# Kernel tuning notes

Measured on AMD Instinct MI355X. Metric: run time of the kernel, lower is better.

Reference implementation:

```python
import jax, jax.numpy as jnp
import numpy as np

NUM_EMBEDDINGS = 2048
EMBEDDING_DIM = 512
INPUT_DIM = 256  # input_chan**2 = 16**2
COMMITMENT_COST = 0.25
BN_EPS = 1e-5


def setup_inputs() -> dict:
    key = jax.random.key(0)
    ks = jax.random.split(key, 8)
    B, N = 64, 1024
    inputs = jax.random.normal(ks[0], (B, N, INPUT_DIM), dtype=jnp.float32)
    # embedding init: uniform(-1/K, 1/K) as in the torch module
    emb_scale = 1.0 / NUM_EMBEDDINGS
    embedding = jax.random.uniform(ks[1], (NUM_EMBEDDINGS, EMBEDDING_DIM), dtype=jnp.float32,
                                   minval=-emb_scale, maxval=emb_scale)
    # Linear layers use torch convention W[out, in]
    W1 = jax.random.normal(ks[2], (EMBEDDING_DIM, INPUT_DIM), dtype=jnp.float32) / np.sqrt(INPUT_DIM)
    b1 = jnp.zeros((EMBEDDING_DIM,), dtype=jnp.float32)
    W2 = jax.random.normal(ks[3], (INPUT_DIM, EMBEDDING_DIM), dtype=jnp.float32) / np.sqrt(EMBEDDING_DIM)
    b2 = jnp.zeros((INPUT_DIM,), dtype=jnp.float32)
    # BatchNorm affine params initialized to 1/0 as in the module
    bn1_gamma = jnp.ones((INPUT_DIM,), dtype=jnp.float32)
    bn1_beta = jnp.zeros((INPUT_DIM,), dtype=jnp.float32)
    bn2_gamma = jnp.ones((EMBEDDING_DIM,), dtype=jnp.float32)
    bn2_beta = jnp.zeros((EMBEDDING_DIM,), dtype=jnp.float32)
    return {"inputs": inputs, "bn1_gamma": bn1_gamma, "bn1_beta": bn1_beta,
            "W1": W1, "b1": b1, "embedding": embedding,
            "bn2_gamma": bn2_gamma, "bn2_beta": bn2_beta, "W2": W2, "b2": b2}


def reference(inputs, bn1_gamma, bn1_beta, W1, b1, embedding, bn2_gamma, bn2_beta, W2, b2):
    sg = jax.lax.stop_gradient
    input_shape = inputs.shape
    flat = inputs.reshape(-1, INPUT_DIM)  # [T, D_in]
    # BatchNorm1d in eval mode (running_mean=0, running_var=1); Dropout is identity in eval.
    bn1_scale = 1.0 / jnp.sqrt(1.0 + BN_EPS)
    x = flat * (bn1_gamma * bn1_scale) + bn1_beta
    x = x @ W1.T + b1  # [T, E]
    # pairwise squared distances to codebook, argmin
    distances = (jnp.sum(x * x, axis=1, keepdims=True)
                 + jnp.sum(embedding * embedding, axis=1)
                 - 2.0 * x @ embedding.T)  # [T, K]
    encoding_indices = jnp.argmin(distances, axis=1)  # [T]
    # gather == one-hot @ embedding (same math, same gradient scatter-add)
    quantized = jnp.take(embedding, encoding_indices, axis=0)  # [T, E]
    bn2_scale = 1.0 / jnp.sqrt(1.0 + BN_EPS)
    quantized = quantized * (bn2_gamma * bn2_scale) + bn2_beta
    quantized = (quantized @ W2.T + b2).reshape(input_shape)
    e_latent_loss = jnp.mean((sg(quantized) - inputs) ** 2)
    q_latent_loss = jnp.mean((quantized - sg(inputs)) ** 2)
    loss = q_latent_loss + COMMITMENT_COST * e_latent_loss
    quantized_st = inputs + sg(quantized - inputs)  # straight-through
    T = flat.shape[0]
    usage = jnp.zeros((NUM_EMBEDDINGS,), dtype=jnp.float32).at[encoding_indices].add(1.0) / T
    return (loss, quantized_st, usage)
```

## Files before the change

### kernel.cpp

```cpp
#include <hip/hip_runtime.h>
#include <math.h>
#include <stdint.h>

#define TOK 65536
#define DIN 256
#define EDIM 512
#define KCB 2048
#define NTA 4096
#define NTB 128

#define OFF_MP   0u
#define OFF_CP   524288u
#define OFF_Q    526336u
#define OFF_W2T  1050624u
#define OFF_U    1181696u
#define OFF_CQ   1182208u
#define OFF_IDX  1182464u
#define OFF_AH   1248000u
#define OFF_BH   5442304u
#define TOT_F    5704448u

typedef short short8 __attribute__((ext_vector_type(8)));
typedef float f32x4 __attribute__((ext_vector_type(4)));

__device__ __forceinline__ unsigned short bf16rne(float x) {
    uint32_t u = __float_as_uint(x);
    u += 0x7fffu + ((u >> 16) & 1u);
    return (unsigned short)(u >> 16);
}
__device__ __forceinline__ void async_load16(const void* g, void* l) {
    __builtin_amdgcn_global_load_lds((const __attribute__((address_space(1))) void*)g,
                                     (__attribute__((address_space(3))) void*)l, 16, 0, 0);
}

__global__ void prep1_kernel(const float* __restrict__ W1, const float* __restrict__ W2,
                             const float* __restrict__ bn1_beta, const float* __restrict__ bn2_gamma,
                             const float* __restrict__ bn2_beta, const float* __restrict__ b2,
                             float* __restrict__ W2T, float* __restrict__ u, float* __restrict__ cQ,
                             float* __restrict__ out) {
    __shared__ float red[256];
    const int b = blockIdx.x, t = threadIdx.x;
    const int gid = b * 256 + t;
    if (gid == 0) out[0] = 0.0f;
    if (gid < KCB) out[1 + TOK * DIN + gid] = 0.0f;
    const float s = 1.0f / sqrtf(1.0f + 1e-5f);
    if (b < EDIM) {
        int e = b;
        W2T[e * DIN + t] = bn2_gamma[e] * s * W2[t * EDIM + e];
        float v = bn1_beta[t] * W1[e * DIN + t];
        red[t] = v; __syncthreads();
        for (int off = 128; off; off >>= 1) { if (t < off) red[t] += red[t + off]; __syncthreads(); }
        if (t == 0) u[e] = red[0];
    } else {
        int o = b - EDIM;
        float v = bn2_beta[t] * W2[o * EDIM + t] + bn2_beta[t + 256] * W2[o * EDIM + t + 256];
        red[t] = v; __syncthreads();
        for (int off = 128; off; off >>= 1) { if (t < off) red[t] += red[t + off]; __syncthreads(); }
        if (t == 0) cQ[o] = b2[o] + red[0];
    }
}

__global__ __launch_bounds__(256) void prep2_kernel(const float* __restrict__ E, const float* __restrict__ W1,
                                                    const float* __restrict__ W2T, const float* __restrict__ bn1_gamma,
                                                    const float* __restrict__ cQ,
                                                    float* __restrict__ Mp, float* __restrict__ Q) {
    __shared__ float Elds[4 * EDIM];
    const int k0 = blockIdx.x * 4, t = threadIdx.x;
    const float4* src = (const float4*)(E + (size_t)k0 * EDIM);
    float4* dst = (float4*)Elds;
    dst[t] = src[t];
    dst[256 + t] = src[256 + t];
    __syncthreads();
    float m[4] = {0, 0, 0, 0};
    float q[4] = {0, 0, 0, 0};
    for (int e0 = 0; e0 < EDIM; e0 += 8) {
        float w1v[8], w2v[8];
#pragma unroll
        for (int j = 0; j < 8; j++) {
            w1v[j] = W1[(e0 + j) * DIN + t];
            w2v[j] = W2T[(e0 + j) * DIN + t];
        }
#pragma unroll
        for (int j = 0; j < 8; j++) {
#pragma unroll
            for (int r = 0; r < 4; r++) {
                float ev = Elds[r * EDIM + e0 + j];
                m[r] += ev * w1v[j]; q[r] += ev * w2v[j];
            }
        }
    }
    const float s = 1.0f / sqrtf(1.0f + 1e-5f);
    const float gs = bn1_gamma[t] * s;
    const float cq = cQ[t];
#pragma unroll
    for (int r = 0; r < 4; r++) {
        Mp[(size_t)(k0 + r) * DIN + t] = gs * m[r];
        Q[(size_t)(k0 + r) * DIN + t] = q[r] + cq;
    }
}

__global__ __launch_bounds__(256) void prep3_packB_kernel(const float* __restrict__ E, const float* __restrict__ b1,
                                                          const float* __restrict__ u, float* __restrict__ cp,
                                                          const float* __restrict__ Mp,
                                                          unsigned short* __restrict__ Bh) {
    __shared__ __align__(16) unsigned short Hs[32 * 264];
    const int t = threadIdx.x, lane = t & 63;
    {
        const int k = blockIdx.x * 4 + (t >> 6);
        const float4* er = (const float4*)(E + (size_t)k * EDIM);
        float sa = 0.0f, sb = 0.0f;
#pragma unroll
        for (int i = 0; i < 2; i++) {
            int j4 = lane * 2 + i;
            float4 ev = er[j4];
            int e = j4 * 4;
            sa += ev.x * (b1[e] + u[e]) + ev.y * (b1[e + 1] + u[e + 1])
                + ev.z * (b1[e + 2] + u[e + 2]) + ev.w * (b1[e + 3] + u[e + 3]);
            sb += ev.x * ev.x + ev.y * ev.y + ev.z * ev.z + ev.w * ev.w;
        }
        float v = sa - 0.5f * sb;
#pragma unroll
        for (int off = 32; off; off >>= 1) v += __shfl_down(v, off, 64);
        if (lane == 0) cp[k] = v;
    }
    if (blockIdx.x >= 64) return;
    const int r0 = blockIdx.x * 32;
    const float4* src = (const float4*)(Mp + (size_t)r0 * DIN);
#pragma unroll
    for (int i = 0; i < 8; i++) {
        int id = i * 256 + t;
        int row = id >> 6, c4 = id & 63;
        float4 v = src[id];
        float f[4] = {v.x, v.y, v.z, v.w};
        ushort4 H;
        unsigned short* hp = (unsigned short*)&H;
#pragma unroll
        for (int j = 0; j < 4; j++) hp[j] = bf16rne(f[j]);
        *(ushort4*)&Hs[row * 264 + c4 * 4] = H;
    }
    __syncthreads();
    const int w = t >> 6;
#pragma unroll
    for (int q = 0; q < 4; q++) {
        int fb = q * 4 + w;
        int tl = fb >> 3, kc = fb & 7;
        int srow = tl * 16 + (lane & 15);
        int scol = kc * 32 + (lane >> 4) * 8;
        short8 vh = *(const short8*)&Hs[srow * 264 + scol];
        size_t off = ((size_t)kc * NTB + (r0 >> 4) + tl) * 512 + lane * 8;
        *(short8*)&Bh[off] = vh;
    }
}

__global__ __launch_bounds__(256) void packA_kernel(const float* __restrict__ X,
                                                    unsigned short* __restrict__ Hp) {
    __shared__ __align__(16) unsigned short Hs[32 * 264];
    const int t = threadIdx.x;
    const int r0 = blockIdx.x * 32;
    const float4* src = (const float4*)(X + (size_t)r0 * DIN);
#pragma unroll
    for (int i = 0; i < 8; i++) {
        int id = i * 256 + t;
        int row = id >> 6, c4 = id & 63;
        float4 v = src[id];
        float f[4] = {v.x, v.y, v.z, v.w};
        ushort4 H;
        unsigned short* hp = (unsigned short*)&H;
#pragma unroll
        for (int j = 0; j < 4; j++) hp[j] = bf16rne(f[j]);
        *(ushort4*)&Hs[row * 264 + c4 * 4] = H;
    }
    __syncthreads();
    const int lane = t & 63, w = t >> 6;
#pragma unroll
    for (int q = 0; q < 4; q++) {
        int fb = q * 4 + w;
        int tl = fb >> 3, kc = fb & 7;
        int srow = tl * 16 + (lane & 15);
        int scol = kc * 32 + (lane >> 4) * 8;
        short8 vh = *(const short8*)&Hs[srow * 264 + scol];
        size_t off = ((size_t)kc * NTA + (r0 >> 4) + tl) * 512 + lane * 8;
        *(short8*)&Hp[off] = vh;
    }
}

__global__ __launch_bounds__(256) void score_mfma_kernel(const unsigned short* __restrict__ Ah,
                                                         const unsigned short* __restrict__ Bh,
                                                         const float* __restrict__ cp,
                                                         int* __restrict__ idxOut) {
    __shared__ __align__(16) unsigned short Blds[2][16 * 512];
    const int t = threadIdx.x, lane = t & 63, w = t >> 6;
    const int m0 = blockIdx.x * 128;
    const int mt0 = (m0 >> 4) + w * 2;
    const int fr = lane & 15;
    const short8* A8 = (const short8*)Ah;

    short8 af[8][2];
#pragma unroll
    for (int kc = 0; kc < 8; kc++)
#pragma unroll
        for (int mt = 0; mt < 2; mt++)
            af[kc][mt] = A8[((size_t)kc * NTA + mt0 + mt) * 64 + lane];

#pragma unroll
    for (int i = 0; i < 4; i++) {
        int tl = i * 4 + w;
        int kc = tl >> 1, nt = tl & 1;
        async_load16(Bh + ((size_t)kc * NTB + nt) * 512 + lane * 8,
                     &Blds[0][tl * 512 + lane * 8]);
    }
    __syncthreads();

    float bestv[2][4];
    int besti[2][4];
#pragma unroll
    for (int mt = 0; mt < 2; mt++)
#pragma unroll
        for (int r = 0; r < 4; r++) { bestv[mt][r] = -3.4e38f; besti[mt][r] = 0; }

#pragma unroll 1
    for (int s = 0; s < 64; s++) {
        const int cur = s & 1;
        if (s < 63) {
            const int nxt = cur ^ 1;
#pragma unroll
            for (int i = 0; i < 4; i++) {
                int tl = i * 4 + w;
                int kc = tl >> 1, nt = tl & 1;
                async_load16(Bh + ((size_t)kc * NTB + (s + 1) * 2 + nt) * 512 + lane * 8,
                             &Blds[nxt][tl * 512 + lane * 8]);
            }
        }
        f32x4 acc[2][2];
#pragma unroll
        for (int mt = 0; mt < 2; mt++)
#pragma unroll
            for (int nt = 0; nt < 2; nt++) acc[mt][nt] = (f32x4){0.f, 0.f, 0.f, 0.f};
#pragma unroll
        for (int kc = 0; kc < 8; kc++) {
            short8 bf0 = *(const short8*)&Blds[cur][(kc * 2 + 0) * 512 + lane * 8];
            short8 bf1 = *(const short8*)&Blds[cur][(kc * 2 + 1) * 512 + lane * 8];
            acc[0][0] = __builtin_amdgcn_mfma_f32_16x16x32_bf16(af[kc][0], bf0, acc[0][0], 0, 0, 0);
            acc[0][1] = __builtin_amdgcn_mfma_f32_16x16x32_bf16(af[kc][0], bf1, acc[0][1], 0, 0, 0);
            acc[1][0] = __builtin_amdgcn_mfma_f32_16x16x32_bf16(af[kc][1], bf0, acc[1][0], 0, 0, 0);
            acc[1][1] = __builtin_amdgcn_mfma_f32_16x16x32_bf16(af[kc][1], bf1, acc[1][1], 0, 0, 0);
        }
        float cpv0 = cp[s * 32 + fr];
        float cpv1 = cp[s * 32 + 16 + fr];
#pragma unroll
        for (int mt = 0; mt < 2; mt++)
#pragma unroll
            for (int r = 0; r < 4; r++) {
                float bv = acc[mt][0][r] + cpv0;
                int bc = s * 32 + fr;
                float v1 = acc[mt][1][r] + cpv1;
                if (v1 > bv) { bv = v1; bc = s * 32 + 16 + fr; }
                if (bv > bestv[mt][r]) { bestv[mt][r] = bv; besti[mt][r] = bc; }
            }
        __syncthreads();
    }
#pragma unroll
    for (int mt = 0; mt < 2; mt++)
#pragma unroll
        for (int r = 0; r < 4; r++) {
            float bv = bestv[mt][r];
            int bc = besti[mt][r];
#pragma unroll
            for (int xm = 1; xm < 16; xm <<= 1) {
                float ov = __shfl_xor(bv, xm, 64);
                int oc = __shfl_xor(bc, xm, 64);
                if (ov > bv || (ov == bv && oc < bc)) { bv = ov; bc = oc; }
            }
            if (fr == 0) {
                int row = m0 + (w * 2 + mt) * 16 + (lane >> 4) * 4 + r;
                idxOut[row] = bc;
            }
        }
}

__global__ __launch_bounds__(256) void gather_out_kernel(const float* __restrict__ flat,
                                                         const float* __restrict__ Q,
                                                         const int* __restrict__ idx,
                                                         float* __restrict__ out) {
    const int t = threadIdx.x;
    const int lane = t & 63;
    const int gw = blockIdx.x * 4 + (t >> 6);
    float lsum = 0.0f;
    for (int r = 0; r < 16; r++) {
        int row = gw * 16 + r;
        int k = idx[row];
        const float* qr = Q + (size_t)k * DIN;
        const float* xr = flat + (size_t)row * DIN;
        float* ob = out + 1 + (size_t)row * DIN;
#pragma unroll
        for (int cc = 0; cc < 4; cc++) {
            int j = lane + 64 * cc;
            float q = qr[j];
            float d = q - xr[j];
            lsum += d * d;
            ob[j] = q;
        }
        if (lane == 0) atomicAdd(out + 1 + TOK * DIN + k, 1.0f / (float)TOK);
    }
#pragma unroll
    for (int off = 32; off; off >>= 1) lsum += __shfl_down(lsum, off, 64);
    if (lane == 0) atomicAdd(out, lsum * (1.25f / (float)((size_t)TOK * DIN)));
}

extern "C" void kernel_launch(void* const* d_in, const int* in_sizes, int n_in,
                              void* d_out, int out_size, void* d_ws, size_t ws_size,
                              hipStream_t stream) {
    const float* inputs = (const float*)d_in[0];
    const float* bn1_gamma = (const float*)d_in[1];
    const float* bn1_beta  = (const float*)d_in[2];
    const float* W1 = (const float*)d_in[3];
    const float* b1 = (const float*)d_in[4];
    const float* E  = (const float*)d_in[5];
    const float* bn2_gamma = (const float*)d_in[6];
    const float* bn2_beta  = (const float*)d_in[7];
    const float* W2 = (const float*)d_in[8];
    const float* b2 = (const float*)d_in[9];

    float* ws = (float*)d_ws;
    float* Mp  = ws + OFF_MP;
    float* cp  = ws + OFF_CP;
    float* Q   = ws + OFF_Q;
    float* W2T = ws + OFF_W2T;
    float* u   = ws + OFF_U;
    float* cQ  = ws + OFF_CQ;
    int* idx   = (int*)(ws + OFF_IDX);
    unsigned short* Ah = (unsigned short*)(ws + OFF_AH);
    unsigned short* Bh = (unsigned short*)(ws + OFF_BH);
    float* out = (float*)d_out;

    hipLaunchKernelGGL(packA_kernel, dim3(TOK / 32), dim3(256), 0, stream, inputs, Ah);
    hipLaunchKernelGGL(prep1_kernel, dim3(768), dim3(256), 0, stream,
                       W1, W2, bn1_beta, bn2_gamma, bn2_beta, b2, W2T, u, cQ, out);
    hipLaunchKernelGGL(prep2_kernel, dim3(512), dim3(256), 0, stream,
                       E, W1, W2T, bn1_gamma, cQ, Mp, Q);
    hipLaunchKernelGGL(prep3_packB_kernel, dim3(512), dim3(256), 0, stream,
                       E, b1, u, cp, Mp, Bh);
    hipLaunchKernelGGL(score_mfma_kernel, dim3(512), dim3(256), 0, stream,
                       Ah, Bh, cp, idx);
    hipLaunchKernelGGL(gather_out_kernel, dim3(1024), dim3(256), 0, stream,
                       inputs, Q, idx, out);
}
```

Baseline: 320.1 us.

## Fuse A packing and gather/loss into the score kernel, widen codebook tile

Removes the separate packA pass by converting each block's input rows to bf16 fragments directly in registers inside the score kernel. The gather/loss/usage step now runs inside the same kernel, with selected indices kept in shared memory. This avoids writing and re-reading the packed A buffer and the index buffer, and drops two launches. The score loop now handles 64 codebook entries per stage instead of 32, which doubles the shared-memory B buffer. Computing cp is merged into prep2 and packB runs as its own small kernel. The trade-off is more registers and LDS per block, which can lower occupancy, and the tail gather loop runs serially after the GEMM.

```diff
diff --git a/kernel.cpp b/kernel.cpp
--- a/kernel.cpp
+++ b/kernel.cpp
@@ -6,7 +6,6 @@
 #define DIN 256
 #define EDIM 512
 #define KCB 2048
-#define NTA 4096
 #define NTB 128
 
 #define OFF_MP   0u
@@ -15,10 +14,8 @@
 #define OFF_W2T  1050624u
 #define OFF_U    1181696u
 #define OFF_CQ   1182208u
-#define OFF_IDX  1182464u
-#define OFF_AH   1248000u
-#define OFF_BH   5442304u
-#define TOT_F    5704448u
+#define OFF_BH   1182464u
+#define TOT_F    1444608u
 
 typedef short short8 __attribute__((ext_vector_type(8)));
 typedef float f32x4 __attribute__((ext_vector_type(4)));
@@ -62,8 +59,10 @@
 
 __global__ __launch_bounds__(256) void prep2_kernel(const float* __restrict__ E, const float* __restrict__ W1,
                                                     const float* __restrict__ W2T, const float* __restrict__ bn1_gamma,
-                                                    const float* __restrict__ cQ,
-                                                    float* __restrict__ Mp, float* __restrict__ Q) {
+                                                    const float* __restrict__ cQ, const float* __restrict__ b1,
+                                                    const float* __restrict__ u,
+                                                    float* __restrict__ Mp, float* __restrict__ Q,
+                                                    float* __restrict__ cp) {
     __shared__ float Elds[4 * EDIM];
     const int k0 = blockIdx.x * 4, t = threadIdx.x;
     const float4* src = (const float4*)(E + (size_t)k0 * EDIM);
@@ -97,33 +96,25 @@
         Mp[(size_t)(k0 + r) * DIN + t] = gs * m[r];
         Q[(size_t)(k0 + r) * DIN + t] = q[r] + cq;
     }
-}
-
-__global__ __launch_bounds__(256) void prep3_packB_kernel(const float* __restrict__ E, const float* __restrict__ b1,
-                                                          const float* __restrict__ u, float* __restrict__ cp,
-                                                          const float* __restrict__ Mp,
-                                                          unsigned short* __restrict__ Bh) {
+    const int r = t >> 6, l = t & 63;
+    float sa = 0.0f, sb = 0.0f;
+#pragma unroll
+    for (int i = 0; i < 8; i++) {
+        int e = l + i * 64;
+        float ev = Elds[r * EDIM + e];
+        float be = b1[e] + u[e];
+        sa += ev * be; sb += ev * ev;
+    }
+    float v = sa - 0.5f * sb;
+#pragma unroll
+    for (int off = 32; off; off >>= 1) v += __shfl_down(v, off, 64);
+    if (l == 0) cp[k0 + r] = v;
+}
+
+__global__ __launch_bounds__(256) void packB_kernel(const float* __restrict__ Mp,
+                                                    unsigned short* __restrict__ Bh) {
     __shared__ __align__(16) unsigned short Hs[32 * 264];
-    const int t = threadIdx.x, lane = t & 63;
-    {
-        const int k = blockIdx.x * 4 + (t >> 6);
-        const float4* er = (const float4*)(E + (size_t)k * EDIM);
-        float sa = 0.0f, sb = 0.0f;
-#pragma unroll
-        for (int i = 0; i < 2; i++) {
-            int j4 = lane * 2 + i;
-            float4 ev = er[j4];
-            int e = j4 * 4;
-            sa += ev.x * (b1[e] + u[e]) + ev.y * (b1[e + 1] + u[e + 1])
-                + ev.z * (b1[e + 2] + u[e + 2]) + ev.w * (b1[e + 3] + u[e + 3]);
-            sb += ev.x * ev.x + ev.y * ev.y + ev.z * ev.z + ev.w * ev.w;
-        }
-        float v = sa - 0.5f * sb;
-#pragma unroll
-        for (int off = 32; off; off >>= 1) v += __shfl_down(v, off, 64);
-        if (lane == 0) cp[k] = v;
-    }
-    if (blockIdx.x >= 64) return;
+    const int t = threadIdx.x, lane = t & 63, w = t >> 6;
     const int r0 = blockIdx.x * 32;
     const float4* src = (const float4*)(Mp + (size_t)r0 * DIN);
 #pragma unroll
@@ -139,7 +130,6 @@
         *(ushort4*)&Hs[row * 264 + c4 * 4] = H;
     }
     __syncthreads();
-    const int w = t >> 6;
 #pragma unroll
     for (int q = 0; q < 4; q++) {
         int fb = q * 4 + w;
@@ -152,60 +142,36 @@
     }
 }
 
-__global__ __launch_bounds__(256) void packA_kernel(const float* __restrict__ X,
-                                                    unsigned short* __restrict__ Hp) {
-    __shared__ __align__(16) unsigned short Hs[32 * 264];
-    const int t = threadIdx.x;
-    const int r0 = blockIdx.x * 32;
-    const float4* src = (const float4*)(X + (size_t)r0 * DIN);
-#pragma unroll
-    for (int i = 0; i < 8; i++) {
-        int id = i * 256 + t;
-        int row = id >> 6, c4 = id & 63;
-        float4 v = src[id];
-        float f[4] = {v.x, v.y, v.z, v.w};
-        ushort4 H;
-        unsigned short* hp = (unsigned short*)&H;
-#pragma unroll
-        for (int j = 0; j < 4; j++) hp[j] = bf16rne(f[j]);
-        *(ushort4*)&Hs[row * 264 + c4 * 4] = H;
-    }
-    __syncthreads();
-    const int lane = t & 63, w = t >> 6;
-#pragma unroll
-    for (int q = 0; q < 4; q++) {
-        int fb = q * 4 + w;
-        int tl = fb >> 3, kc = fb & 7;
-        int srow = tl * 16 + (lane & 15);
-        int scol = kc * 32 + (lane >> 4) * 8;
-        short8 vh = *(const short8*)&Hs[srow * 264 + scol];
-        size_t off = ((size_t)kc * NTA + (r0 >> 4) + tl) * 512 + lane * 8;
-        *(short8*)&Hp[off] = vh;
-    }
-}
-
-__global__ __launch_bounds__(256) void score_mfma_kernel(const unsigned short* __restrict__ Ah,
-                                                         const unsigned short* __restrict__ Bh,
-                                                         const float* __restrict__ cp,
-                                                         int* __restrict__ idxOut) {
-    __shared__ __align__(16) unsigned short Blds[2][16 * 512];
+__global__ __launch_bounds__(256) void score_fused_kernel(const float* __restrict__ flat,
+                                                          const unsigned short* __restrict__ Bh,
+                                                          const float* __restrict__ cp,
+                                                          const float* __restrict__ Q,
+                                                          float* __restrict__ out) {
+    __shared__ __align__(16) unsigned short Blds[2][32 * 512];
+    __shared__ int ksel[128];
     const int t = threadIdx.x, lane = t & 63, w = t >> 6;
     const int m0 = blockIdx.x * 128;
-    const int mt0 = (m0 >> 4) + w * 2;
-    const int fr = lane & 15;
-    const short8* A8 = (const short8*)Ah;
+    const int fr = lane & 15, qr = lane >> 4;
 
     short8 af[8][2];
 #pragma unroll
     for (int kc = 0; kc < 8; kc++)
 #pragma unroll
-        for (int mt = 0; mt < 2; mt++)
-            af[kc][mt] = A8[((size_t)kc * NTA + mt0 + mt) * 64 + lane];
-
-#pragma unroll
-    for (int i = 0; i < 4; i++) {
+        for (int mt = 0; mt < 2; mt++) {
+            int row = m0 + w * 32 + mt * 16 + fr;
+            const float* p = flat + (size_t)row * DIN + kc * 32 + qr * 8;
+            float4 a = *(const float4*)p;
+            float4 b = *(const float4*)(p + 4);
+            float f[8] = {a.x, a.y, a.z, a.w, b.x, b.y, b.z, b.w};
+            unsigned short* hp = (unsigned short*)&af[kc][mt];
+#pragma unroll
+            for (int j = 0; j < 8; j++) hp[j] = bf16rne(f[j]);
+        }
+
+#pragma unroll
+    for (int i = 0; i < 8; i++) {
         int tl = i * 4 + w;
-        int kc = tl >> 1, nt = tl & 1;
+        int kc = tl >> 2, nt = tl & 3;
         async_load16(Bh + ((size_t)kc * NTB + nt) * 512 + lane * 8,
                      &Blds[0][tl * 512 + lane * 8]);
     }
@@ -218,47 +184,66 @@
 #pragma unroll
         for (int r = 0; r < 4; r++) { bestv[mt][r] = -3.4e38f; besti[mt][r] = 0; }
 
+    const f32x4 ZERO4 = {0.f, 0.f, 0.f, 0.f};
+
 #pragma unroll 1
-    for (int s = 0; s < 64; s++) {
+    for (int s = 0; s < 32; s++) {
         const int cur = s & 1;
-        if (s < 63) {
+        if (s < 31) {
             const int nxt = cur ^ 1;
 #pragma unroll
-            for (int i = 0; i < 4; i++) {
+            for (int i = 0; i < 8; i++) {
                 int tl = i * 4 + w;
-                int kc = tl >> 1, nt = tl & 1;
-                async_load16(Bh + ((size_t)kc * NTB + (s + 1) * 2 + nt) * 512 + lane * 8,
+                int kc = tl >> 2, nt = tl & 3;
+                async_load16(Bh + ((size_t)kc * NTB + (s + 1) * 4 + nt) * 512 + lane * 8,
                              &Blds[nxt][tl * 512 + lane * 8]);
             }
         }
-        f32x4 acc[2][2];
+        f32x4 acc[2][4];
+        {
+            short8 bf[4];
+#pragma unroll
+            for (int nt = 0; nt < 4; nt++)
+                bf[nt] = *(const short8*)&Blds[cur][nt * 512 + lane * 8];
+#pragma unroll
+            for (int mt = 0; mt < 2; mt++)
+#pragma unroll
+                for (int nt = 0; nt < 4; nt++)
+                    acc[mt][nt] = __builtin_amdgcn_mfma_f32_16x16x32_bf16(af[0][mt], bf[nt], ZERO4, 0, 0, 0);
+        }
+#pragma unroll
+        for (int kc = 1; kc < 8; kc++) {
+            short8 bf[4];
+#pragma unroll
+            for (int nt = 0; nt < 4; nt++)
+                bf[nt] = *(const short8*)&Blds[cur][(kc * 4 + nt) * 512 + lane * 8];
+#pragma unroll
+            for (int mt = 0; mt < 2; mt++)
+#pragma unroll
+                for (int nt = 0; nt < 4; nt++)
+                    acc[mt][nt] = __builtin_amdgcn_mfma_f32_16x16x32_bf16(af[kc][mt], bf[nt], acc[mt][nt], 0, 0, 0);
+        }
+        const int base = s * 64 + fr;
+        float cpv[4];
+        int cidx[4];
+#pragma unroll
+        for (int nt = 0; nt < 4; nt++) { cpv[nt] = cp[base + nt * 16]; cidx[nt] = base + nt * 16; }
 #pragma unroll
         for (int mt = 0; mt < 2; mt++)
 #pragma unroll
-            for (int nt = 0; nt < 2; nt++) acc[mt][nt] = (f32x4){0.f, 0.f, 0.f, 0.f};
-#pragma unroll
-        for (int kc = 0; kc < 8; kc++) {
-            short8 bf0 = *(const short8*)&Blds[cur][(kc * 2 + 0) * 512 + lane * 8];
-            short8 bf1 = *(const short8*)&Blds[cur][(kc * 2 + 1) * 512 + lane * 8];
-            acc[0][0] = __builtin_amdgcn_mfma_f32_16x16x32_bf16(af[kc][0], bf0, acc[0][0], 0, 0, 0);
-            acc[0][1] = __builtin_amdgcn_mfma_f32_16x16x32_bf16(af[kc][0], bf1, acc[0][1], 0, 0, 0);
-            acc[1][0] = __builtin_amdgcn_mfma_f32_16x16x32_bf16(af[kc][1], bf0, acc[1][0], 0, 0, 0);
-            acc[1][1] = __builtin_amdgcn_mfma_f32_16x16x32_bf16(af[kc][1], bf1, acc[1][1], 0, 0, 0);
-        }
-        float cpv0 = cp[s * 32 + fr];
-        float cpv1 = cp[s * 32 + 16 + fr];
-#pragma unroll
-        for (int mt = 0; mt < 2; mt++)
-#pragma unroll
             for (int r = 0; r < 4; r++) {
-                float bv = acc[mt][0][r] + cpv0;
-                int bc = s * 32 + fr;
-                float v1 = acc[mt][1][r] + cpv1;
-                if (v1 > bv) { bv = v1; bc = s * 32 + 16 + fr; }
-                if (bv > bestv[mt][r]) { bestv[mt][r] = bv; besti[mt][r] = bc; }
+                float v = acc[mt][0][r] + cpv[0];
+                int ci = cidx[0];
+#pragma unroll
+                for (int nt = 1; nt < 4; nt++) {
+                    float vi = acc[mt][nt][r] + cpv[nt];
+                    if (vi > v) { v = vi; ci = cidx[nt]; }
+                }
+                if (v > bestv[mt][r]) { bestv[mt][r] = v; besti[mt][r] = ci; }
             }
         __syncthreads();
     }
+
 #pragma unroll
     for (int mt = 0; mt < 2; mt++)
 #pragma unroll
@@ -271,31 +256,22 @@
                 int oc = __shfl_xor(bc, xm, 64);
                 if (ov > bv || (ov == bv && oc < bc)) { bv = ov; bc = oc; }
             }
-            if (fr == 0) {
-                int row = m0 + (w * 2 + mt) * 16 + (lane >> 4) * 4 + r;
-                idxOut[row] = bc;
-            }
-        }
-}
-
-__global__ __launch_bounds__(256) void gather_out_kernel(const float* __restrict__ flat,
-                                                         const float* __restrict__ Q,
-                                                         const int* __restrict__ idx,
-                                                         float* __restrict__ out) {
-    const int t = threadIdx.x;
-    const int lane = t & 63;
-    const int gw = blockIdx.x * 4 + (t >> 6);
+            if (fr == 0) ksel[w * 32 + mt * 16 + qr * 4 + r] = bc;
+        }
+    __syncthreads();
+
     float lsum = 0.0f;
-    for (int r = 0; r < 16; r++) {
-        int row = gw * 16 + r;
-        int k = idx[row];
-        const float* qr = Q + (size_t)k * DIN;
+    for (int rr = 0; rr < 32; rr++) {
+        int rl = w * 32 + rr;
+        int row = m0 + rl;
+        int k = ksel[rl];
+        const float* qr_ = Q + (size_t)k * DIN;
         const float* xr = flat + (size_t)row * DIN;
         float* ob = out + 1 + (size_t)row * DIN;
 #pragma unroll
         for (int cc = 0; cc < 4; cc++) {
             int j = lane + 64 * cc;
-            float q = qr[j];
+            float q = qr_[j];
             float d = q - xr[j];
             lsum += d * d;
             ob[j] = q;
@@ -328,20 +304,14 @@
     float* W2T = ws + OFF_W2T;
     float* u   = ws + OFF_U;
     float* cQ  = ws + OFF_CQ;
-    int* idx   = (int*)(ws + OFF_IDX);
-    unsigned short* Ah = (unsigned short*)(ws + OFF_AH);
     unsigned short* Bh = (unsigned short*)(ws + OFF_BH);
     float* out = (float*)d_out;
 
-    hipLaunchKernelGGL(packA_kernel, dim3(TOK / 32), dim3(256), 0, stream, inputs, Ah);
     hipLaunchKernelGGL(prep1_kernel, dim3(768), dim3(256), 0, stream,
                        W1, W2, bn1_beta, bn2_gamma, bn2_beta, b2, W2T, u, cQ, out);
     hipLaunchKernelGGL(prep2_kernel, dim3(512), dim3(256), 0, stream,
-                       E, W1, W2T, bn1_gamma, cQ, Mp, Q);
-    hipLaunchKernelGGL(prep3_packB_kernel, dim3(512), dim3(256), 0, stream,
-                       E, b1, u, cp, Mp, Bh);
-    hipLaunchKernelGGL(score_mfma_kernel, dim3(512), dim3(256), 0, stream,
-                       Ah, Bh, cp, idx);
-    hipLaunchKernelGGL(gather_out_kernel, dim3(1024), dim3(256), 0, stream,
-                       inputs, Q, idx, out);
-}
+                       E, W1, W2T, bn1_gamma, cQ, b1, u, Mp, Q, cp);
+    hipLaunchKernelGGL(packB_kernel, dim3(64), dim3(256), 0, stream, Mp, Bh);
+    hipLaunchKernelGGL(score_fused_kernel, dim3(512), dim3(256), 0, stream,
+                       inputs, Bh, cp, Q, out);
+}
```

New measurement: 278.5 us. 1.15x faster.
